# Kernel tuning notes

Hardware: AMD Instinct MI355X
Metric: run time of the kernel (lower is better)

Reference implementation:

```python
import jax, jax.numpy as jnp
import numpy as np

H_DIM = 768
NUM_HEADS = 12
HEAD_DIM = H_DIM // NUM_HEADS
ROPE_BASE = 10000.0


def rope_cos_sin(seq_len, dim):
    inv_freq = 1.0 / (ROPE_BASE ** (jnp.arange(0, dim, 2, dtype=jnp.float32) / dim))
    t = jnp.arange(seq_len, dtype=jnp.float32)
    freqs = jnp.outer(t, inv_freq)              # [seq, dim/2]
    emb = jnp.concatenate([freqs, freqs], axis=-1)  # [seq, dim]
    return jnp.cos(emb), jnp.sin(emb)


def rotate_half(x):
    x1, x2 = jnp.split(x, 2, axis=-1)
    return jnp.concatenate([-x2, x1], axis=-1)


def setup_inputs() -> dict:
    key = jax.random.key(0)
    ks = jax.random.split(key, 9)
    s = 1.0 / np.sqrt(H_DIM)
    inp = {
        'x': jax.random.normal(ks[0], (2, 8, 1024, H_DIM), dtype=jnp.float32),
        'Wq': jax.random.normal(ks[1], (H_DIM, H_DIM), dtype=jnp.float32) * s,
        'bq': jnp.zeros((H_DIM,), dtype=jnp.float32),
        'Wk': jax.random.normal(ks[2], (H_DIM, H_DIM), dtype=jnp.float32) * s,
        'bk': jnp.zeros((H_DIM,), dtype=jnp.float32),
        'Wv': jax.random.normal(ks[3], (H_DIM, H_DIM), dtype=jnp.float32) * s,
        'bv': jnp.zeros((H_DIM,), dtype=jnp.float32),
        'Wo': jax.random.normal(ks[4], (H_DIM, H_DIM), dtype=jnp.float32) * s,
        'bo': jnp.zeros((H_DIM,), dtype=jnp.float32),
        'mask': jnp.ones((2, 8, 1, 1, 1024), dtype=jnp.int32),
    }
    return inp


def reference(x, Wq, bq, Wk, bk, Wv, bv, Wo, bo, mask):
    b, r, s, d = x.shape
    H, D = NUM_HEADS, HEAD_DIM

    def proj(W, bvec):
        # [b,r,s,d] -> [b,r,H,s,D]
        y = x @ W + bvec
        return y.reshape(b, r, s, H, D).transpose(0, 1, 3, 2, 4)

    q = proj(Wq, bq)
    k = proj(Wk, bk)
    v = proj(Wv, bv)

    cos, sin = rope_cos_sin(s, D)   # [s, D]
    cos = cos[None, None, None]     # broadcast over b,r,H
    sin = sin[None, None, None]
    q = q * cos + rotate_half(q) * sin
    k = k * cos + rotate_half(k) * sin

    scores = jnp.einsum('brhqd,brhkd->brhqk', q, k) / jnp.sqrt(jnp.float32(D))
    scores = jnp.where(mask == 0, -jnp.inf, scores)
    probs = jax.nn.softmax(scores, axis=-1)  # dropout is identity in eval
    out = jnp.einsum('brhqk,brhkd->brhqd', probs, v)
    out = out.transpose(0, 1, 3, 2, 4).reshape(b, r, s, d)
    return out @ Wo + bo
```

## Files before the change

kernel.cpp:

```cpp
#include <hip/hip_runtime.h>


#define M_TOT 16384
#define DM    768
#define NH    12
#define HD    64
#define SEQ   1024

typedef __attribute__((ext_vector_type(8))) __bf16 bf16x8;
typedef __attribute__((ext_vector_type(4))) __bf16 bf16x4;
typedef __attribute__((ext_vector_type(4))) short s16x4;
typedef __attribute__((ext_vector_type(4))) float  f32x4;

static __device__ __forceinline__ unsigned short f2b(float f) {
  unsigned u = __builtin_bit_cast(unsigned, f);
  u += 0x7FFFu + ((u >> 16) & 1u);
  return (unsigned short)(u >> 16);
}
static __device__ __forceinline__ float b2f(unsigned short s) {
  unsigned u = ((unsigned)s) << 16;
  return __builtin_bit_cast(float, u);
}
static __device__ __forceinline__ unsigned cvt_pk_bf16(float lo, float hi) {
  unsigned d;
  asm("v_cvt_pk_bf16_f32 %0, %1, %2" : "=v"(d) : "v"(lo), "v"(hi));
  return d;
}

static __device__ __forceinline__ f32x4 mfma16(uint2 a, uint2 b, f32x4 c) {
#if __has_builtin(__builtin_amdgcn_mfma_f32_16x16x16_bf16)
  union U { uint2 u; bf16x4 v; } A, B;
  A.u = a; B.u = b;
  return __builtin_amdgcn_mfma_f32_16x16x16_bf16(A.v, B.v, c, 0, 0, 0);
#else
  union U { uint2 u; s16x4 v; } A, B;
  A.u = a; B.u = b;
  return __builtin_amdgcn_mfma_f32_16x16x16bf16_1k(A.v, B.v, c, 0, 0, 0);
#endif
}

static __device__ __forceinline__ void gl_lds16(const void* g, void* l) {
  __builtin_amdgcn_global_load_lds(
      (const __attribute__((address_space(1))) unsigned*)g,
      (__attribute__((address_space(3))) unsigned*)l, 16, 0, 0);
}

static __device__ __forceinline__ int swz_src(int c) {
  return ((c >> 3) << 6) + (((c & 7) ^ ((c >> 3) & 7)) << 3);
}
static __device__ __forceinline__ int swz_rd(int row, int col16) {
  return (row << 6) + ((col16 ^ (row & 7)) << 3);
}

__global__ void cvt_x(const float* __restrict__ x, unsigned short* __restrict__ xb) {
  const int n4 = M_TOT * DM / 4;
  for (int i = blockIdx.x * blockDim.x + threadIdx.x; i < n4; i += gridDim.x * blockDim.x) {
    float4 v = ((const float4*)x)[i];
    ushort4 o;
    o.x = f2b(v.x); o.y = f2b(v.y); o.z = f2b(v.z); o.w = f2b(v.w);
    ((ushort4*)xb)[i] = o;
  }
}

__global__ void prep_w(const float* __restrict__ Wq, const float* __restrict__ Wk,
                       const float* __restrict__ Wv, const float* __restrict__ Wo,
                       unsigned short* __restrict__ Wt) {
  __shared__ float T[64][65];
  const int wsel = blockIdx.z;
  const float* W = wsel == 0 ? Wq : wsel == 1 ? Wk : wsel == 2 ? Wv : Wo;
  const int k0 = blockIdx.x * 64, n0 = blockIdx.y * 64;
  const int t = threadIdx.x;
#pragma unroll
  for (int p = 0; p < 16; ++p) {
    int e = p * 256 + t, r = e >> 6, c = e & 63;
    T[r][c] = W[(size_t)(k0 + r) * DM + n0 + c];
  }
  __syncthreads();
  unsigned short* dst = Wt + (size_t)wsel * DM * DM;
#pragma unroll
  for (int p = 0; p < 16; ++p) {
    int e = p * 256 + t, r = e >> 6, c = e & 63;
    dst[(size_t)(n0 + r) * DM + k0 + c] = f2b(T[c][r]);
  }
}

__global__ void rope_tab(float* __restrict__ cosT, float* __restrict__ sinT) {
  int i = blockIdx.x * blockDim.x + threadIdx.x;
  int s = i >> 5, j = i & 31;
  float inv = powf(10000.0f, -(float)j * (1.0f / 32.0f));
  float ang = (float)s * inv;
  cosT[i] = cosf(ang);
  sinT[i] = sinf(ang);
}

__global__ void bias_cat(const float* __restrict__ bq, const float* __restrict__ bk,
                         const float* __restrict__ bv, float* __restrict__ bcat) {
  int i = blockIdx.x * 256 + threadIdx.x;
  if (i < 3 * DM)
    bcat[i] = i < DM ? bq[i] : (i < 2 * DM ? bk[i - DM] : bv[i - 2 * DM]);
}

static __device__ __forceinline__ void gemm_core(const unsigned short* __restrict__ A,
                                                 const unsigned short* __restrict__ Bt,
                                                 int m0, int n0, f32x4 acc[4][4],
                                                 char* smem) {
  unsigned short* As = (unsigned short*)smem;
  unsigned short* Bs = As + 128 * 64;
  const int tid = threadIdx.x, lane = tid & 63, w = tid >> 6;
  const int wr = w >> 1, wc = w & 1;
  const int lr = lane & 15, g4 = lane >> 4;

#pragma unroll
  for (int i = 0; i < 4; ++i)
#pragma unroll
    for (int j = 0; j < 4; ++j) acc[i][j] = (f32x4){0.f, 0.f, 0.f, 0.f};

  for (int kt = 0; kt < DM / 64; ++kt) {
    const int k0 = kt * 64;
#pragma unroll
    for (int p = 0; p < 4; ++p) {
      int cb = p * 256 + w * 64;
      int c = cb + lane;
      const int ro = c >> 3;
      const int co = ((c & 7) ^ (ro & 7)) << 3;
      gl_lds16(A + (size_t)(m0 + ro) * DM + k0 + co, (char*)As + cb * 16);
      gl_lds16(Bt + (size_t)(n0 + ro) * DM + k0 + co, (char*)Bs + cb * 16);
    }
    __syncthreads();
#pragma unroll
    for (int kk = 0; kk < 2; ++kk) {
      const int ch = kk * 4 + g4;
      bf16x8 a[4], b[4];
#pragma unroll
      for (int i = 0; i < 4; ++i) {
        const int row = wr * 64 + i * 16 + lr;
        a[i] = *(const bf16x8*)&As[(row << 6) + ((ch ^ (row & 7)) << 3)];
      }
#pragma unroll
      for (int j = 0; j < 4; ++j) {
        const int row = wc * 64 + j * 16 + lr;
        b[j] = *(const bf16x8*)&Bs[(row << 6) + ((ch ^ (row & 7)) << 3)];
      }
#pragma unroll
      for (int i = 0; i < 4; ++i)
#pragma unroll
        for (int j = 0; j < 4; ++j)
          acc[i][j] = __builtin_amdgcn_mfma_f32_16x16x32_bf16(a[i], b[j], acc[i][j], 0, 0, 0);
    }
    __syncthreads();
  }
}

__global__ __launch_bounds__(256, 4) void gemm_qkv(
    const unsigned short* __restrict__ xb, const unsigned short* __restrict__ Wt,
    const float* __restrict__ bcat, const float* __restrict__ cosT,
    const float* __restrict__ sinT, unsigned short* __restrict__ Qh,
    unsigned short* __restrict__ Kh, unsigned short* __restrict__ Vt) {
  __shared__ alignas(16) char smem[32768];
  const int id = blockIdx.x;
  const int xcdc = id & 7, rem = id >> 3;
  const int y = rem % 18, xc = rem / 18;
  const int xm = xc * 8 + xcdc;
  const int m0 = xm * 128, n0 = y * 128;
  f32x4 acc[4][4];
  gemm_core(xb, Wt, m0, n0, acc, smem);

  const int tid = threadIdx.x, lane = tid & 63, w = tid >> 6;
  const int wr = w >> 1, wc = w & 1;
  const int lr = lane & 15, g4 = lane >> 4;
  const int zone = y / 6;
  const int wcol0 = n0 - zone * DM + wc * 64;
  const int h = wcol0 >> 6;
  const int br = m0 >> 10;
  const int s_base = (m0 & 1023) + wr * 64;

  if (zone == 2) {
    unsigned short* dstb = Vt + ((size_t)(br * NH + h) * HD) * SEQ;
#pragma unroll
    for (int j = 0; j < 4; ++j) {
      const int d = j * 16 + lr;
      const float bv = bcat[n0 + wc * 64 + d];
#pragma unroll
      for (int i = 0; i < 4; ++i) {
        const int s0 = s_base + i * 16 + g4 * 4;
        ushort4 st;
        st.x = f2b(acc[i][j][0] + bv);
        st.y = f2b(acc[i][j][1] + bv);
        st.z = f2b(acc[i][j][2] + bv);
        st.w = f2b(acc[i][j][3] + bv);
        *(ushort4*)&dstb[(size_t)d * SEQ + s0] = st;
      }
    }
  } else {
    const float sc = zone == 0 ? 0.125f * 1.44269504f : 1.0f;
    unsigned short* dstb = (zone ? Kh : Qh) + ((size_t)(br * NH + h) * SEQ) * HD;
    char* Wb = smem + (size_t)w * 8192;
    const int s_q = s_base + lane;
    const int bcol = n0 + wc * 64;

#pragma unroll
    for (int hh = 0; hh < 2; ++hh) {
#pragma unroll
      for (int jj = 0; jj < 2; ++jj) {
        const int jp = hh + jj * 2;
        const float bv = bcat[bcol + jp * 16 + lr];
        const int dslot = jj * 16 + lr;
        const int sub = (dslot & 3) * 4;
        const int ch = dslot >> 2;
#pragma unroll
        for (int i = 0; i < 4; ++i) {
#pragma unroll
          for (int r = 0; r < 4; ++r) {
            const int s_loc = i * 16 + g4 * 4 + r;
            *(float*)(Wb + s_loc * 128 + ((ch ^ (s_loc & 7)) << 4) + sub) =
                (acc[i][jp][r] + bv) * sc;
          }
        }
      }
      unsigned short* drow = dstb + (size_t)s_q * HD + hh * 16;
      const char* Rb = Wb + lane * 128;
      const int lx = lane & 7;
#pragma unroll
      for (int c = 0; c < 4; ++c) {
        f32x4 va = *(const f32x4*)(Rb + ((c ^ lx) << 4));
        f32x4 vb = *(const f32x4*)(Rb + (((c + 4) ^ lx) << 4));
        float4 c4 = *(const float4*)&cosT[s_q * 32 + hh * 16 + c * 4];
        float4 s4 = *(const float4*)&sinT[s_q * 32 + hh * 16 + c * 4];
        uint2 oa, ob;
        oa.x = cvt_pk_bf16(va[0] * c4.x - vb[0] * s4.x, va[1] * c4.y - vb[1] * s4.y);
        oa.y = cvt_pk_bf16(va[2] * c4.z - vb[2] * s4.z, va[3] * c4.w - vb[3] * s4.w);
        ob.x = cvt_pk_bf16(vb[0] * c4.x + va[0] * s4.x, vb[1] * c4.y + va[1] * s4.y);
        ob.y = cvt_pk_bf16(vb[2] * c4.z + va[2] * s4.z, vb[3] * c4.w + va[3] * s4.w);
        *(uint2*)(drow + c * 4)      = oa;
        *(uint2*)(drow + 32 + c * 4) = ob;
      }
    }
  }
}

__global__ __launch_bounds__(256, 4) void gemm_o(const unsigned short* __restrict__ attnb,
                                                 const unsigned short* __restrict__ WtO,
                                                 const float* __restrict__ bo,
                                                 float* __restrict__ out) {
  __shared__ alignas(16) char smem[32768];
  const int id = blockIdx.x;
  const int xcdc = id & 7, rem = id >> 3;
  const int y = rem % 6, xc = rem / 6;
  const int m0 = (xc * 8 + xcdc) * 128, n0 = y * 128;
  f32x4 acc[4][4];
  gemm_core(attnb, WtO, m0, n0, acc, smem);
  const int tid = threadIdx.x, lane = tid & 63, w = tid >> 6;
  const int wr = w >> 1, wc = w & 1;
  const int lr = lane & 15, g4 = lane >> 4;
#pragma unroll
  for (int j = 0; j < 4; ++j) {
    const int col = n0 + wc * 64 + j * 16 + lr;
    const float bv = bo[col];
#pragma unroll
    for (int i = 0; i < 4; ++i) {
      const int rowb = m0 + wr * 64 + i * 16 + g4 * 4;
#pragma unroll
      for (int r = 0; r < 4; ++r)
        out[(size_t)(rowb + r) * DM + col] = acc[i][j][r] + bv;
    }
  }
}

__global__ __launch_bounds__(256) void attn_fwd(const unsigned short* __restrict__ Qh,
                                                const unsigned short* __restrict__ Kh,
                                                const unsigned short* __restrict__ Vt,
                                                const int* __restrict__ mask,
                                                unsigned short* __restrict__ attnb) {
  __shared__ unsigned short Ks[2][64 * 64];
  __shared__ unsigned short Vs[2][64 * 64];
  const int id = blockIdx.x;
  const int xcdc = id & 7, rem = id >> 3;
  const int qt = rem & 15, g = rem >> 4;
  const int brh = g * 8 + xcdc;
  const int br = brh / NH, h = brh - br * NH;
  const int tid = threadIdx.x, lane = tid & 63, w = tid >> 6;
  const int lr = lane & 15, g4 = lane >> 4;

  const unsigned short* Kg = Kh + (size_t)brh * SEQ * HD;
  const unsigned short* Vg = Vt + (size_t)brh * HD * SEQ;
  const int* mrow0 = mask + (size_t)br * SEQ + g4 * 4;

  int4 mi = *(const int4*)&mask[(size_t)br * SEQ + tid * 4];
  const int allLive = __syncthreads_and(mi.x && mi.y && mi.z && mi.w);

#pragma unroll
  for (int p = 0; p < 2; ++p) {
    int cb = p * 256 + w * 64;
    int c = cb + lane;
    gl_lds16(Kg + swz_src(c), (char*)Ks[0] + cb * 16);
    gl_lds16(Vg + (size_t)(c >> 3) * SEQ + (((c & 7) ^ ((c >> 3) & 7)) << 3),
             (char*)Vs[0] + cb * 16);
  }

  const unsigned short* Qg = Qh + ((size_t)brh * SEQ + qt * 64 + w * 16 + lr) * HD;
  bf16x8 qa[2];
  qa[0] = *(const bf16x8*)(Qg + g4 * 8);
  qa[1] = *(const bf16x8*)(Qg + 32 + g4 * 8);

  f32x4 o[4], lacc;
#pragma unroll
  for (int j = 0; j < 4; ++j) o[j] = (f32x4){0.f, 0.f, 0.f, 0.f};
  lacc = (f32x4){0.f, 0.f, 0.f, 0.f};
  const uint2 ones = {0x3F803F80u, 0x3F803F80u};

  __syncthreads();

  unsigned short* KsC = Ks[0];
  unsigned short* VsC = Vs[0];
  unsigned short* KsN = Ks[1];
  unsigned short* VsN = Vs[1];

  for (int kb = 0; kb < SEQ / 64; ++kb) {
    if (kb + 1 < SEQ / 64) {
#pragma unroll
      for (int p = 0; p < 2; ++p) {
        int cb = p * 256 + w * 64;
        int c = cb + lane;
        gl_lds16(Kg + (size_t)(kb + 1) * 64 * HD + swz_src(c), (char*)KsN + cb * 16);
        gl_lds16(Vg + (size_t)(c >> 3) * SEQ + (kb + 1) * 64 +
                     (((c & 7) ^ ((c >> 3) & 7)) << 3),
                 (char*)VsN + cb * 16);
      }
    }

    f32x4 s4[4];
#pragma unroll
    for (int j = 0; j < 4; ++j) s4[j] = (f32x4){0.f, 0.f, 0.f, 0.f};
    __builtin_amdgcn_s_setprio(1);
#pragma unroll
    for (int kk = 0; kk < 2; ++kk) {
#pragma unroll
      for (int j = 0; j < 4; ++j) {
        bf16x8 kf = *(const bf16x8*)&KsC[swz_rd(j * 16 + lr, kk * 4 + g4)];
        s4[j] = __builtin_amdgcn_mfma_f32_16x16x32_bf16(kf, qa[kk], s4[j], 0, 0, 0);
      }
    }
    __builtin_amdgcn_s_setprio(0);

    if (!allLive) {
      const int* mr = mrow0 + kb * 64;
#pragma unroll
      for (int j = 0; j < 4; ++j) {
        int4 mq = *(const int4*)&mr[j * 16];
        s4[j][0] += mq.x ? 0.f : -3e38f;
        s4[j][1] += mq.y ? 0.f : -3e38f;
        s4[j][2] += mq.z ? 0.f : -3e38f;
        s4[j][3] += mq.w ? 0.f : -3e38f;
      }
    }

    uint2 wb[4];
#pragma unroll
    for (int j = 0; j < 4; ++j) {
      wb[j].x = cvt_pk_bf16(exp2f(s4[j][0]), exp2f(s4[j][1]));
      wb[j].y = cvt_pk_bf16(exp2f(s4[j][2]), exp2f(s4[j][3]));
    }

    __builtin_amdgcn_s_setprio(1);
#pragma unroll
    for (int j = 0; j < 4; ++j) lacc = mfma16(ones, wb[j], lacc);
#pragma unroll
    for (int jj = 0; jj < 4; ++jj) {
      const int row = jj * 16 + lr;
#pragma unroll
      for (int j = 0; j < 4; ++j) {
        const int c8 = j * 4 + g4;
        uint2 av = *(const uint2*)&VsC[(row << 6) + ((((c8 >> 1) ^ (lr & 7))) << 3) +
                                       ((c8 & 1) << 2)];
        o[jj] = mfma16(av, wb[j], o[jj]);
      }
    }
    __builtin_amdgcn_s_setprio(0);

    __syncthreads();
    unsigned short* t;
    t = KsC; KsC = KsN; KsN = t;
    t = VsC; VsC = VsN; VsN = t;
  }

  float l = lacc[0];
  float inv = l > 0.f ? 1.0f / l : 0.f;
  unsigned short* dst =
      attnb + ((size_t)(br * SEQ + qt * 64 + w * 16 + lr)) * DM + h * HD;
#pragma unroll
  for (int j = 0; j < 4; ++j) {
    ushort4 st;
    st.x = f2b(o[j][0] * inv);
    st.y = f2b(o[j][1] * inv);
    st.z = f2b(o[j][2] * inv);
    st.w = f2b(o[j][3] * inv);
    *(ushort4*)&dst[j * 16 + g4 * 4] = st;
  }
}

extern "C" void kernel_launch(void* const* d_in, const int* in_sizes, int n_in,
                              void* d_out, int out_size, void* d_ws, size_t ws_size,
                              hipStream_t stream) {
  const float* x  = (const float*)d_in[0];
  const float* Wq = (const float*)d_in[1];
  const float* bq = (const float*)d_in[2];
  const float* Wk = (const float*)d_in[3];
  const float* bk = (const float*)d_in[4];
  const float* Wv = (const float*)d_in[5];
  const float* bv = (const float*)d_in[6];
  const float* Wo = (const float*)d_in[7];
  const float* bo = (const float*)d_in[8];
  const int* mask = (const int*)d_in[9];
  float* out = (float*)d_out;

  const size_t OFF_XB   = 0;
  const size_t OFF_WT   = 25165824;
  const size_t OFF_COS  = 29884416;
  const size_t OFF_SIN  = 30015488;
  const size_t OFF_BC   = 30146560;
  const size_t OFF_ATT  = 30158848;
  const size_t OFF_QH   = 55324672;
  const size_t OFF_KH   = 80490496;
  const size_t OFF_VT   = 105656320;
  const size_t REQUIRED = 130822144;
  if (ws_size < REQUIRED) return;

  char* w = (char*)d_ws;
  unsigned short* xb   = (unsigned short*)(w + OFF_XB);
  unsigned short* Wt   = (unsigned short*)(w + OFF_WT);
  float* cosT          = (float*)(w + OFF_COS);
  float* sinT          = (float*)(w + OFF_SIN);
  float* bcat          = (float*)(w + OFF_BC);
  unsigned short* attnb = (unsigned short*)(w + OFF_ATT);
  unsigned short* Qh   = (unsigned short*)(w + OFF_QH);
  unsigned short* Kh   = (unsigned short*)(w + OFF_KH);
  unsigned short* Vt   = (unsigned short*)(w + OFF_VT);

  cvt_x<<<2048, 256, 0, stream>>>(x, xb);
  prep_w<<<dim3(12, 12, 4), 256, 0, stream>>>(Wq, Wk, Wv, Wo, Wt);
  rope_tab<<<128, 256, 0, stream>>>(cosT, sinT);
  bias_cat<<<9, 256, 0, stream>>>(bq, bk, bv, bcat);
  gemm_qkv<<<2304, 256, 0, stream>>>(xb, Wt, bcat, cosT, sinT, Qh, Kh, Vt);
  attn_fwd<<<3072, 256, 0, stream>>>(Qh, Kh, Vt, mask, attnb);
  gemm_o<<<768, 256, 0, stream>>>(attnb, Wt + (size_t)3 * DM * DM, bo, out);
}
```

Measured before the change: 240.6 us.

## Overlap next-tile LDS loads with MFMA in GEMM core and merge prep kernels

Restructures the GEMM main loop so the second half-tile fragments are read into registers, then the next K-tile's global-to-LDS copy is issued before the remaining MFMAs, overlapping memory traffic with matrix math. MFMA sections are wrapped in raised wave priority. The weight transpose, RoPE table and bias concat kernels are fused into a single launch to cut launch overhead. Extra register fragments may raise register pressure under the existing occupancy bound.

Measured after the change: 236.1 us. About the same (-1.9%).

```diff
diff --git a/kernel.cpp b/kernel.cpp
--- a/kernel.cpp
+++ b/kernel.cpp
@@ -62,42 +62,43 @@
   }
 }
 
-__global__ void prep_w(const float* __restrict__ Wq, const float* __restrict__ Wk,
-                       const float* __restrict__ Wv, const float* __restrict__ Wo,
-                       unsigned short* __restrict__ Wt) {
+__global__ void prep(const float* __restrict__ Wq, const float* __restrict__ Wk,
+                     const float* __restrict__ Wv, const float* __restrict__ Wo,
+                     unsigned short* __restrict__ Wt,
+                     float* __restrict__ cosT, float* __restrict__ sinT,
+                     const float* __restrict__ bq, const float* __restrict__ bk,
+                     const float* __restrict__ bv, float* __restrict__ bcat) {
   __shared__ float T[64][65];
-  const int wsel = blockIdx.z;
-  const float* W = wsel == 0 ? Wq : wsel == 1 ? Wk : wsel == 2 ? Wv : Wo;
-  const int k0 = blockIdx.x * 64, n0 = blockIdx.y * 64;
+  const int bid = blockIdx.x;
   const int t = threadIdx.x;
-#pragma unroll
-  for (int p = 0; p < 16; ++p) {
-    int e = p * 256 + t, r = e >> 6, c = e & 63;
-    T[r][c] = W[(size_t)(k0 + r) * DM + n0 + c];
-  }
-  __syncthreads();
-  unsigned short* dst = Wt + (size_t)wsel * DM * DM;
-#pragma unroll
-  for (int p = 0; p < 16; ++p) {
-    int e = p * 256 + t, r = e >> 6, c = e & 63;
-    dst[(size_t)(n0 + r) * DM + k0 + c] = f2b(T[c][r]);
-  }
-}
-
-__global__ void rope_tab(float* __restrict__ cosT, float* __restrict__ sinT) {
-  int i = blockIdx.x * blockDim.x + threadIdx.x;
-  int s = i >> 5, j = i & 31;
-  float inv = powf(10000.0f, -(float)j * (1.0f / 32.0f));
-  float ang = (float)s * inv;
-  cosT[i] = cosf(ang);
-  sinT[i] = sinf(ang);
-}
-
-__global__ void bias_cat(const float* __restrict__ bq, const float* __restrict__ bk,
-                         const float* __restrict__ bv, float* __restrict__ bcat) {
-  int i = blockIdx.x * 256 + threadIdx.x;
-  if (i < 3 * DM)
-    bcat[i] = i < DM ? bq[i] : (i < 2 * DM ? bk[i - DM] : bv[i - 2 * DM]);
+  if (bid < 576) {
+    const int wsel = bid / 144, r144 = bid % 144;
+    const int k0 = (r144 % 12) * 64, n0 = (r144 / 12) * 64;
+    const float* W = wsel == 0 ? Wq : wsel == 1 ? Wk : wsel == 2 ? Wv : Wo;
+#pragma unroll
+    for (int p = 0; p < 16; ++p) {
+      int e = p * 256 + t, r = e >> 6, c = e & 63;
+      T[r][c] = W[(size_t)(k0 + r) * DM + n0 + c];
+    }
+    __syncthreads();
+    unsigned short* dst = Wt + (size_t)wsel * DM * DM;
+#pragma unroll
+    for (int p = 0; p < 16; ++p) {
+      int e = p * 256 + t, r = e >> 6, c = e & 63;
+      dst[(size_t)(n0 + r) * DM + k0 + c] = f2b(T[c][r]);
+    }
+  } else if (bid < 704) {
+    int i = (bid - 576) * 256 + t;
+    int s = i >> 5, j = i & 31;
+    float inv = powf(10000.0f, -(float)j * (1.0f / 32.0f));
+    float ang = (float)s * inv;
+    cosT[i] = cosf(ang);
+    sinT[i] = sinf(ang);
+  } else {
+    int i = (bid - 704) * 256 + t;
+    if (i < 3 * DM)
+      bcat[i] = i < DM ? bq[i] : (i < 2 * DM ? bk[i - DM] : bv[i - 2 * DM]);
+  }
 }
 
 static __device__ __forceinline__ void gemm_core(const unsigned short* __restrict__ A,
@@ -115,8 +116,7 @@
 #pragma unroll
     for (int j = 0; j < 4; ++j) acc[i][j] = (f32x4){0.f, 0.f, 0.f, 0.f};
 
-  for (int kt = 0; kt < DM / 64; ++kt) {
-    const int k0 = kt * 64;
+  auto STAGE = [&](int k0) {
 #pragma unroll
     for (int p = 0; p < 4; ++p) {
       int cb = p * 256 + w * 64;
@@ -126,11 +126,15 @@
       gl_lds16(A + (size_t)(m0 + ro) * DM + k0 + co, (char*)As + cb * 16);
       gl_lds16(Bt + (size_t)(n0 + ro) * DM + k0 + co, (char*)Bs + cb * 16);
     }
-    __syncthreads();
-#pragma unroll
-    for (int kk = 0; kk < 2; ++kk) {
-      const int ch = kk * 4 + g4;
-      bf16x8 a[4], b[4];
+  };
+
+  STAGE(0);
+  __syncthreads();
+
+  for (int kt = 0; kt < DM / 64; ++kt) {
+    bf16x8 a[4], b[4];
+    {
+      const int ch = g4;
 #pragma unroll
       for (int i = 0; i < 4; ++i) {
         const int row = wr * 64 + i * 16 + lr;
@@ -141,12 +145,37 @@
         const int row = wc * 64 + j * 16 + lr;
         b[j] = *(const bf16x8*)&Bs[(row << 6) + ((ch ^ (row & 7)) << 3)];
       }
+      __builtin_amdgcn_s_setprio(1);
 #pragma unroll
       for (int i = 0; i < 4; ++i)
 #pragma unroll
         for (int j = 0; j < 4; ++j)
           acc[i][j] = __builtin_amdgcn_mfma_f32_16x16x32_bf16(a[i], b[j], acc[i][j], 0, 0, 0);
-    }
+      __builtin_amdgcn_s_setprio(0);
+    }
+    bf16x8 a1[4], b1[4];
+    {
+      const int ch = 4 + g4;
+#pragma unroll
+      for (int i = 0; i < 4; ++i) {
+        const int row = wr * 64 + i * 16 + lr;
+        a1[i] = *(const bf16x8*)&As[(row << 6) + ((ch ^ (row & 7)) << 3)];
+      }
+#pragma unroll
+      for (int j = 0; j < 4; ++j) {
+        const int row = wc * 64 + j * 16 + lr;
+        b1[j] = *(const bf16x8*)&Bs[(row << 6) + ((ch ^ (row & 7)) << 3)];
+      }
+    }
+    __syncthreads();
+    if (kt + 1 < DM / 64) STAGE((kt + 1) * 64);
+    __builtin_amdgcn_s_setprio(1);
+#pragma unroll
+    for (int i = 0; i < 4; ++i)
+#pragma unroll
+      for (int j = 0; j < 4; ++j)
+        acc[i][j] = __builtin_amdgcn_mfma_f32_16x16x32_bf16(a1[i], b1[j], acc[i][j], 0, 0, 0);
+    __builtin_amdgcn_s_setprio(0);
     __syncthreads();
   }
 }
@@ -437,9 +466,7 @@
   unsigned short* Vt   = (unsigned short*)(w + OFF_VT);
 
   cvt_x<<<2048, 256, 0, stream>>>(x, xb);
-  prep_w<<<dim3(12, 12, 4), 256, 0, stream>>>(Wq, Wk, Wv, Wo, Wt);
-  rope_tab<<<128, 256, 0, stream>>>(cosT, sinT);
-  bias_cat<<<9, 256, 0, stream>>>(bq, bk, bv, bcat);
+  prep<<<713, 256, 0, stream>>>(Wq, Wk, Wv, Wo, Wt, cosT, sinT, bq, bk, bv, bcat);
   gemm_qkv<<<2304, 256, 0, stream>>>(xb, Wt, bcat, cosT, sinT, Qh, Kh, Vt);
   attn_fwd<<<3072, 256, 0, stream>>>(Qh, Kh, Vt, mask, attnb);
   gemm_o<<<768, 256, 0, stream>>>(attnb, Wt + (size_t)3 * DM * DM, bo, out);
```
